# Kernel optimization log

Hardware: AMD Instinct MI355X
Metric: run time of the kernel (lower is better)

## Reference

```python
import jax, jax.numpy as jnp
import numpy as np

B, N, D, H = 1, 4096, 1024, 16
HD = D // H  # head_dim = 64


def setup_inputs() -> dict:
    key = jax.random.key(0)
    ks = jax.random.split(key, 5)
    s = 0.02
    return {
        "x": jax.random.normal(ks[0], (B, N, D), dtype=jnp.float32),
        "Wq": jax.random.normal(ks[1], (D, D), dtype=jnp.float32) * s,
        "Wk": jax.random.normal(ks[2], (D, D), dtype=jnp.float32) * s,
        "Wv": jax.random.normal(ks[3], (D, D), dtype=jnp.float32) * s,
        "Wo": jax.random.normal(ks[4], (D, D), dtype=jnp.float32) * s,
        "bo": jnp.zeros((D,), dtype=jnp.float32),
    }


def reference(x, Wq, Wk, Wv, Wo, bo):
    b, n, d = x.shape
    # QKV projections -> [b, h, n, hd]
    def proj(W):
        return jnp.einsum("bnd,de->bne", x, W).reshape(b, n, H, HD).transpose(0, 2, 1, 3)
    q, k, v = proj(Wq), proj(Wk), proj(Wv)
    # Scores [b, h, n, n] with causal mask (matches masked_fill with triu(diag=1))
    scores = jnp.einsum("bhqd,bhkd->bhqk", q, k)
    causal = jnp.tril(jnp.ones((n, n), dtype=bool))
    scores = jnp.where(causal, scores, -jnp.inf)
    attn = jax.nn.softmax(scores / jnp.sqrt(jnp.float32(HD)), axis=-1)
    # dropout p=0.0 -> identity
    ctx = jnp.einsum("bhqk,bhkd->bhqd", attn, v)
    ctx = ctx.transpose(0, 2, 1, 3).reshape(b, n, d)
    return jnp.einsum("bnd,de->bne", ctx, Wo) + bo
```

## Files before the change

kernel.cpp:

```cpp
#include <hip/hip_runtime.h>


#define N_TOK 4096
#define DMODEL 1024
#define NH 16
#define HDIM 64

typedef __bf16 bf16x8 __attribute__((ext_vector_type(8)));
typedef __bf16 bf16x2v __attribute__((ext_vector_type(2)));
typedef short short4v __attribute__((ext_vector_type(4)));
typedef unsigned int uint2v __attribute__((ext_vector_type(2)));
typedef float f32x4 __attribute__((ext_vector_type(4)));

__device__ __forceinline__ unsigned short f2bf(float f) {
  unsigned u = __builtin_bit_cast(unsigned, f);
  u += 0x7FFFu + ((u >> 16) & 1u);
  return (unsigned short)(u >> 16);
}

__device__ __forceinline__ float bf2f(unsigned short u) {
  unsigned x = (unsigned)u << 16;
  return __builtin_bit_cast(float, x);
}

__device__ __forceinline__ unsigned pack2bf(float f0, float f1) {
  unsigned a = __builtin_bit_cast(unsigned, f0);
  unsigned b = __builtin_bit_cast(unsigned, f1);
  a += 0x7FFFu + ((a >> 16) & 1u);
  b += 0x7FFFu + ((b >> 16) & 1u);
  return (a >> 16) | (b & 0xFFFF0000u);
}

__device__ __forceinline__ unsigned packpk(float f0, float f1) {
#if defined(__HIP_DEVICE_COMPILE__) && __has_builtin(__builtin_amdgcn_cvt_pk_bf16_f32)
  bf16x2v r = __builtin_amdgcn_cvt_pk_bf16_f32(f0, f1);
  return __builtin_bit_cast(unsigned, r);
#else
  return pack2bf(f0, f1);
#endif
}

__device__ __forceinline__ float fast_exp2(float x) {
#if defined(__HIP_DEVICE_COMPILE__)
#if __has_builtin(__builtin_amdgcn_exp2f)
  return __builtin_amdgcn_exp2f(x);
#else
  float r;
  asm("v_exp_f32 %0, %1" : "=v"(r) : "v"(x));
  return r;
#endif
#else
  return exp2f(x);
#endif
}

__device__ __forceinline__ f32x4 mfma16x16x16(short4v a, short4v b, f32x4 c) {
#if defined(__HIP_DEVICE_COMPILE__)
#if __has_builtin(__builtin_amdgcn_mfma_f32_16x16x16bf16_1k)
  return __builtin_amdgcn_mfma_f32_16x16x16bf16_1k(a, b, c, 0, 0, 0);
#else
  asm volatile("v_mfma_f32_16x16x16_bf16 %0, %1, %2, %0\n\ts_nop 7\n\ts_nop 1"
               : "+v"(c) : "v"(a), "v"(b));
  return c;
#endif
#else
  return c;
#endif
}

__device__ __forceinline__ void gll16(const unsigned short* g, unsigned short* l) {
#if defined(__HIP_DEVICE_COMPILE__)
  __builtin_amdgcn_global_load_lds((const __attribute__((address_space(1))) void*)g,
                                   (__attribute__((address_space(3))) void*)l, 16, 0, 0);
#endif
}

__global__ __launch_bounds__(256) void prep_kernel(
    const float* __restrict__ x, unsigned short* __restrict__ xb,
    const float* __restrict__ Wq, const float* __restrict__ Wk,
    const float* __restrict__ Wv, const float* __restrict__ Wo,
    unsigned short* __restrict__ Wqt, unsigned short* __restrict__ Wkt,
    unsigned short* __restrict__ Wvt, unsigned short* __restrict__ Wot) {
  const int bx = blockIdx.x;
  if (bx < 4096) {
    const int i = (bx * 256 + threadIdx.x) * 4;
    float4 v = *(const float4*)(x + i);
    ushort4 o;
    o.x = f2bf(v.x); o.y = f2bf(v.y); o.z = f2bf(v.z); o.w = f2bf(v.w);
    *(ushort4*)(xb + i) = o;
    return;
  }
  __shared__ float t[32][33];
  const int r = bx - 4096;
  const int z = r >> 10, rem = r & 1023;
  const int by = rem >> 5, bxx = rem & 31;
  const float* src;
  unsigned short* dst;
  switch (z) {
    case 0: src = Wq; dst = Wqt; break;
    case 1: src = Wk; dst = Wkt; break;
    case 2: src = Wv; dst = Wvt; break;
    default: src = Wo; dst = Wot; break;
  }
  const int tx = threadIdx.x & 31, ty = threadIdx.x >> 5;
  const int xx = bxx * 32 + tx;
  const int y0 = by * 32;
#pragma unroll
  for (int i = 0; i < 32; i += 8) t[ty + i][tx] = src[(y0 + ty + i) * DMODEL + xx];
  __syncthreads();
  const int ox = by * 32 + tx;
  const int oy0 = bxx * 32;
#pragma unroll
  for (int i = 0; i < 32; i += 8) dst[(oy0 + ty + i) * DMODEL + ox] = f2bf(t[tx][ty + i]);
}

__global__ __launch_bounds__(256) void gemm_qkv_kernel(
    const unsigned short* __restrict__ xb,
    const unsigned short* __restrict__ Wqt, const unsigned short* __restrict__ Wkt,
    const unsigned short* __restrict__ Wvt,
    unsigned short* __restrict__ Qg, unsigned short* __restrict__ Kg,
    unsigned short* __restrict__ Vtg) {
  __shared__ unsigned short As[128 * 32];
  __shared__ unsigned short Bs[128 * 32];
  __shared__ unsigned short Tt[64 * 132];
  const int z = blockIdx.z;
  const unsigned short* Bmat = (z == 0) ? Wqt : ((z == 1) ? Wkt : Wvt);
  const int tid = threadIdx.x, lane = tid & 63, wv = tid >> 6;
  const int quad = lane >> 4, l15 = lane & 15;
  const int wm = wv >> 1, wn = wv & 1;
  const int tm0 = blockIdx.y * 128, tn0 = blockIdx.x * 128;
  const int lrow = lane >> 2, lcol = (lane & 3) * 8;
  const f32x4 zero4 = {0.f, 0.f, 0.f, 0.f};
  f32x4 acc[4][4];
#pragma unroll
  for (int i = 0; i < 4; ++i)
#pragma unroll
    for (int j = 0; j < 4; ++j) acc[i][j] = zero4;

  for (int kb = 0; kb < DMODEL; kb += 32) {
#pragma unroll
    for (int r = 0; r < 2; ++r) {
      const int row0 = r * 64 + wv * 16;
      gll16(&xb[(tm0 + row0 + lrow) * DMODEL + kb + lcol], &As[row0 * 32]);
      gll16(&Bmat[(tn0 + row0 + lrow) * DMODEL + kb + lcol], &Bs[row0 * 32]);
    }
    __syncthreads();
    bf16x8 af[4], bfr[4];
#pragma unroll
    for (int i = 0; i < 4; ++i) {
      af[i]  = *(const bf16x8*)&As[(wm * 64 + i * 16 + l15) * 32 + quad * 8];
      bfr[i] = *(const bf16x8*)&Bs[(wn * 64 + i * 16 + l15) * 32 + quad * 8];
    }
#pragma unroll
    for (int mt = 0; mt < 4; ++mt)
#pragma unroll
      for (int nt = 0; nt < 4; ++nt)
        acc[mt][nt] = __builtin_amdgcn_mfma_f32_16x16x32_bf16(af[mt], bfr[nt], acc[mt][nt], 0, 0, 0);
    __syncthreads();
  }

  const float qs = 0.125f * 1.44269504088896f;
  if (z < 2) {
#pragma unroll
    for (int mt = 0; mt < 4; ++mt)
#pragma unroll
      for (int nt = 0; nt < 4; ++nt)
#pragma unroll
        for (int r = 0; r < 4; ++r) {
          const int row = tm0 + wm * 64 + mt * 16 + quad * 4 + r;
          const int col = tn0 + wn * 64 + nt * 16 + l15;
          const float v = acc[mt][nt][r];
          const int hh = col >> 6, hd = col & 63;
          if (z == 0) Qg[(hh * N_TOK + row) * HDIM + hd] = f2bf(v * qs);
          else        Kg[(hh * N_TOK + row) * HDIM + hd] = f2bf(v);
        }
  } else {
#pragma unroll 1
    for (int p = 0; p < 2; ++p) {
      if (wn == p) {
#pragma unroll
        for (int mt = 0; mt < 4; ++mt)
#pragma unroll
          for (int nt = 0; nt < 4; ++nt) {
            const int c = nt * 16 + l15;
#pragma unroll
            for (int r = 0; r < 4; ++r)
              Tt[c * 132 + wm * 64 + mt * 16 + quad * 4 + r] = f2bf(acc[mt][nt][r]);
          }
      }
      __syncthreads();
      const int c = tid >> 2, seg = tid & 3;
      const int hh = (tn0 + p * 64) >> 6;
      unsigned short* dst = Vtg + hh * (HDIM * N_TOK) + c * N_TOK + tm0 + seg * 32;
      const unsigned short* srcp = &Tt[c * 132 + seg * 32];
#pragma unroll
      for (int j = 0; j < 4; ++j)
        *(uint4*)(dst + j * 8) = *(const uint4*)(srcp + j * 8);
      __syncthreads();
    }
  }
}

#define TRW 68

__device__ static const unsigned char T_TAB[80] = {
    7, 14, 15, 15, 21, 22, 22, 23, 23, 23, 28, 29, 29, 30, 30, 30, 31, 31, 31, 31,
    6, 12, 13, 13, 14, 18, 19, 19, 20, 20, 20, 21, 21, 22, 24, 25, 25, 26, 26, 26,
    27, 27, 27, 27, 28, 28, 28, 29, 29, 30,
    5, 10, 11, 11, 12, 16, 16, 17, 17, 17, 18, 18, 19, 24, 24, 24, 25, 25, 26,
    4, 8, 9, 9, 10, 16,
    3, 8,
    2,
    1,
    0};
__device__ static const unsigned char G_TAB[80] = {
    0, 0, 0, 1, 0, 0, 1, 0, 1, 2, 0, 0, 1, 0, 1, 2, 0, 1, 2, 3,
    0, 0, 0, 1, 1, 0, 0, 1, 0, 1, 2, 1, 2, 2, 0, 0, 1, 0, 1, 2,
    0, 1, 2, 3, 1, 2, 3, 2, 3, 3,
    0, 0, 0, 1, 1, 0, 1, 0, 1, 2, 1, 2, 2, 1, 2, 3, 2, 3, 3,
    0, 0, 0, 1, 1, 2,
    0, 1,
    0,
    0,
    0};
__device__ static const unsigned char PS_TAB[32] = {
    0, 0, 0, 0, 0, 0, 0, 0,
    0, 2, 4, 6, 8, 10, 12, 14,
    16, 19, 22, 25, 28, 31, 34, 37,
    40, 44, 48, 52, 56, 60, 64, 68};

__device__ __forceinline__ unsigned short* part_slot_ptr(
    unsigned short* poA, unsigned short* poB, int slot) {
  return (slot < 384) ? poA + (size_t)slot * 8192
                      : poB + (size_t)(slot - 384) * 8192;
}

__device__ __forceinline__ void stage_kv(
    const unsigned short* __restrict__ Kh, const unsigned short* __restrict__ Vh,
    int kv0, char* buf, int wv, int lane) {
  unsigned short* Ksb = (unsigned short*)buf;
  unsigned short* Vsb = (unsigned short*)(buf + 8192);
  const int r8 = lane >> 3, g = lane & 7;
  const int sw = ((g ^ r8) * 8);
  const int row = wv * 8;
  gll16(&Kh[(kv0 + row + r8) * HDIM + sw], &Ksb[row * 64]);
  gll16(&Vh[(row + r8) * N_TOK + kv0 + sw], &Vsb[row * 64]);
}

template <bool MASKED>
__device__ __forceinline__ void attn_step(
    int kvs, int qw, int quad, int l15,
    const unsigned short* __restrict__ Ks, const unsigned short* __restrict__ Vs,
    const bf16x8 (&qf)[2], f32x4 (&o)[4], float& l_) {
  const f32x4 zero4 = {0.f, 0.f, 0.f, 0.f};
  const int s = l15 & 7;
  const int g0 = (quad ^ s) * 8;
  f32x4 c[4];
#pragma unroll
  for (int mt = 0; mt < 4; ++mt) {
    const unsigned short* kp = &Ks[(mt * 16 + l15) * 64];
    const bf16x8 kf0 = *(const bf16x8*)(kp + g0);
    const bf16x8 kf1 = *(const bf16x8*)(kp + (g0 ^ 32));
    c[mt] = __builtin_amdgcn_mfma_f32_16x16x32_bf16(kf0, qf[0], zero4, 0, 0, 0);
    c[mt] = __builtin_amdgcn_mfma_f32_16x16x32_bf16(kf1, qf[1], c[mt], 0, 0, 0);
  }
  short4v pb[4];
  const int q = qw + l15;
  float ls = 0.f;
#pragma unroll
  for (int mt = 0; mt < 4; ++mt) {
    float p[4];
#pragma unroll
    for (int r = 0; r < 4; ++r) {
      float v = c[mt][r];
      if (MASKED) v = ((kvs + mt * 16 + quad * 4 + r) <= q) ? v : -3e38f;
      p[r] = fast_exp2(v);
    }
    ls += (p[0] + p[1]) + (p[2] + p[3]);
    uint2v w;
    w.x = packpk(p[0], p[1]);
    w.y = packpk(p[2], p[3]);
    pb[mt] = __builtin_bit_cast(short4v, w);
  }
  l_ += ls;
#pragma unroll
  for (int mt = 0; mt < 4; ++mt)
#pragma unroll
    for (int dt = 0; dt < 4; ++dt) {
      const int gv = (((2 * mt + (quad >> 1)) ^ s) * 8) + (quad & 1) * 4;
      const short4v vfx = *(const short4v*)&Vs[(dt * 16 + l15) * 64 + gv];
      o[dt] = mfma16x16x16(vfx, pb[mt], o[dt]);
    }
}

__global__ __launch_bounds__(512, 8) void attn_kernel(
    const unsigned short* __restrict__ Qg, const unsigned short* __restrict__ Kg,
    const unsigned short* __restrict__ Vtg, unsigned short* __restrict__ ctx,
    unsigned short* __restrict__ part_oA, unsigned short* __restrict__ part_oB,
    float* __restrict__ part_l) {
  __shared__ __align__(16) char smem[34816];
  const int tid = threadIdx.x, lane = tid & 63, wv = tid >> 6;
  const int quad = lane >> 4, l15 = lane & 15;

  const int xcd = blockIdx.x & 7;
  const int iblk = blockIdx.x >> 3;
  const int h = (xcd << 1) | (iblk & 1);
  const int u = iblk >> 1;
  const int t = T_TAB[u], g = G_TAB[u];
  const int ng = (t >> 3) + 1;
  const int tp1 = t + 1;
  const int gbase = tp1 / ng;
  const int grem = tp1 - gbase * ng;
  const int s0 = g * gbase + (g < grem ? g : grem);
  const int cnt = gbase + (g < grem ? 1 : 0);
  const int mlen = 2 * cnt;
  const bool multi = (t >= 8);
  const int qb = t * 128, qw = qb + wv * 16;

  const unsigned short* Qh = Qg + h * N_TOK * HDIM;
  const unsigned short* Kh = Kg + h * N_TOK * HDIM;
  const unsigned short* Vh = Vtg + h * HDIM * N_TOK;

  bf16x8 qf[2];
#pragma unroll
  for (int hh = 0; hh < 2; ++hh)
    qf[hh] = *(const bf16x8*)&Qh[(qw + l15) * HDIM + hh * 32 + quad * 8];

  const f32x4 zero4 = {0.f, 0.f, 0.f, 0.f};
  f32x4 o[4];
#pragma unroll
  for (int dt = 0; dt < 4; ++dt) o[dt] = zero4;
  float l_ = 0.f;

  const int kvbase = s0 << 7;
  stage_kv(Kh, Vh, kvbase, smem, wv, lane);
  stage_kv(Kh, Vh, kvbase + 64, smem + 16384, wv, lane);
  int cur = 0;
#pragma unroll 1
  for (int mc = 0; mc < mlen; ++mc) {
    const int kv0 = kvbase + mc * 64;
    if (mc + 1 < mlen) asm volatile("s_waitcnt vmcnt(2)" ::: "memory");
    else               asm volatile("s_waitcnt vmcnt(0)" ::: "memory");
    __builtin_amdgcn_s_barrier();
    const unsigned short* Ksb = (const unsigned short*)(smem + cur * 16384);
    const unsigned short* Vsb = (const unsigned short*)(smem + cur * 16384 + 8192);
    if (kv0 <= qw + 15) {
      __builtin_amdgcn_s_setprio(1);
      if (kv0 + 63 <= qw)
        attn_step<false>(kv0, qw, quad, l15, Ksb, Vsb, qf, o, l_);
      else
        attn_step<true>(kv0, qw, quad, l15, Ksb, Vsb, qf, o, l_);
      __builtin_amdgcn_s_setprio(0);
    }
    if (mc + 2 < mlen) {
      __builtin_amdgcn_s_barrier();
      stage_kv(Kh, Vh, kv0 + 128, smem + cur * 16384, wv, lane);
    }
    cur ^= 1;
  }
  __syncthreads();

  float* Tr = (float*)(smem + wv * (16 * TRW * 4));
  const int tq = lane >> 2, seg = lane & 3;
  if (!multi) {
    float l = l_;
    l += __shfl_xor(l, 16, 64);
    l += __shfl_xor(l, 32, 64);
    const float inv = 1.0f / l;
#pragma unroll
    for (int dt = 0; dt < 4; ++dt) {
      f32x4 v = o[dt] * inv;
      *(f32x4*)&Tr[l15 * TRW + dt * 16 + quad * 4] = v;
    }
    unsigned short* dst = &ctx[(qb + wv * 16 + tq) * DMODEL + h * HDIM + seg * 16];
    const float* src = &Tr[tq * TRW + seg * 16];
#pragma unroll
    for (int j = 0; j < 2; ++j) {
      const float* s8 = src + j * 8;
      uint4 w;
      w.x = pack2bf(s8[0], s8[1]);
      w.y = pack2bf(s8[2], s8[3]);
      w.z = pack2bf(s8[4], s8[5]);
      w.w = pack2bf(s8[6], s8[7]);
      *(uint4*)(dst + j * 8) = w;
    }
  } else {
    const int slot = h * 72 + PS_TAB[t] + g;
    float l = l_;
    l += __shfl_xor(l, 16, 64);
    l += __shfl_xor(l, 32, 64);
    if (quad == 0) part_l[slot * 128 + wv * 16 + l15] = l;
#pragma unroll
    for (int dt = 0; dt < 4; ++dt)
      *(f32x4*)&Tr[l15 * TRW + dt * 16 + quad * 4] = o[dt];
    unsigned short* dst = part_slot_ptr(part_oA, part_oB, slot) +
                          (wv * 16 + tq) * 64 + seg * 16;
    const float* src = &Tr[tq * TRW + seg * 16];
#pragma unroll
    for (int j = 0; j < 2; ++j) {
      const float* s8 = src + j * 8;
      uint4 w;
      w.x = pack2bf(s8[0], s8[1]);
      w.y = pack2bf(s8[2], s8[3]);
      w.z = pack2bf(s8[4], s8[5]);
      w.w = pack2bf(s8[6], s8[7]);
      *(uint4*)(dst + j * 8) = w;
    }
  }
}

__global__ __launch_bounds__(256) void merge_kernel(
    unsigned short* __restrict__ part_oA, unsigned short* __restrict__ part_oB,
    const float* __restrict__ part_l, unsigned short* __restrict__ ctx) {
  const int b = blockIdx.x;
  const int h = b / 24, tt = b - h * 24;
  const int t = tt + 8;
  const int ng = (t >> 3) + 1;
  const int tid = threadIdx.x;
  const int q = tid >> 1, half = tid & 1;
  const int slot0 = h * 72 + PS_TAB[t];
  float l = 0.f;
  for (int g = 0; g < ng; ++g) l += part_l[(slot0 + g) * 128 + q];
  const float inv = 1.0f / l;
  unsigned short* dst = &ctx[(t * 128 + q) * DMODEL + h * HDIM + half * 32];
#pragma unroll
  for (int j = 0; j < 4; ++j) {
    float acc[8] = {0.f, 0.f, 0.f, 0.f, 0.f, 0.f, 0.f, 0.f};
    for (int g = 0; g < ng; ++g) {
      const unsigned short* po = part_slot_ptr(part_oA, part_oB, slot0 + g);
      const uint4 w = *(const uint4*)(po + q * 64 + half * 32 + j * 8);
      const unsigned short* us = (const unsigned short*)&w;
#pragma unroll
      for (int e = 0; e < 8; ++e) acc[e] += bf2f(us[e]);
    }
    uint4 w;
    w.x = pack2bf(acc[0] * inv, acc[1] * inv);
    w.y = pack2bf(acc[2] * inv, acc[3] * inv);
    w.z = pack2bf(acc[4] * inv, acc[5] * inv);
    w.w = pack2bf(acc[6] * inv, acc[7] * inv);
    *(uint4*)(dst + j * 8) = w;
  }
}

__global__ __launch_bounds__(256) void gemm_out_kernel(
    const unsigned short* __restrict__ ctxb, const unsigned short* __restrict__ Wot,
    const float* __restrict__ bo, float* __restrict__ out) {
  __shared__ unsigned short As[128 * 32];
  __shared__ unsigned short Bs[128 * 32];
  const int tid = threadIdx.x, lane = tid & 63, wv = tid >> 6;
  const int quad = lane >> 4, l15 = lane & 15;
  const int wm = wv >> 1, wn = wv & 1;
  const int tm0 = blockIdx.y * 128, tn0 = blockIdx.x * 128;
  const int lrow = lane >> 2, lcol = (lane & 3) * 8;
  const f32x4 zero4 = {0.f, 0.f, 0.f, 0.f};
  f32x4 acc[4][4];
#pragma unroll
  for (int i = 0; i < 4; ++i)
#pragma unroll
    for (int j = 0; j < 4; ++j) acc[i][j] = zero4;

  for (int kb = 0; kb < DMODEL; kb += 32) {
#pragma unroll
    for (int r = 0; r < 2; ++r) {
      const int row0 = r * 64 + wv * 16;
      gll16(&ctxb[(tm0 + row0 + lrow) * DMODEL + kb + lcol], &As[row0 * 32]);
      gll16(&Wot[(tn0 + row0 + lrow) * DMODEL + kb + lcol], &Bs[row0 * 32]);
    }
    __syncthreads();
    bf16x8 af[4], bfr[4];
#pragma unroll
    for (int i = 0; i < 4; ++i) {
      af[i]  = *(const bf16x8*)&As[(wm * 64 + i * 16 + l15) * 32 + quad * 8];
      bfr[i] = *(const bf16x8*)&Bs[(wn * 64 + i * 16 + l15) * 32 + quad * 8];
    }
#pragma unroll
    for (int mt = 0; mt < 4; ++mt)
#pragma unroll
      for (int nt = 0; nt < 4; ++nt)
        acc[mt][nt] = __builtin_amdgcn_mfma_f32_16x16x32_bf16(af[mt], bfr[nt], acc[mt][nt], 0, 0, 0);
    __syncthreads();
  }
#pragma unroll
  for (int mt = 0; mt < 4; ++mt)
#pragma unroll
    for (int nt = 0; nt < 4; ++nt)
#pragma unroll
      for (int r = 0; r < 4; ++r) {
        const int row = tm0 + wm * 64 + mt * 16 + quad * 4 + r;
        const int col = tn0 + wn * 64 + nt * 16 + l15;
        out[row * DMODEL + col] = acc[mt][nt][r] + bo[col];
      }
}

extern "C" void kernel_launch(void* const* d_in, const int* in_sizes, int n_in,
                              void* d_out, int out_size, void* d_ws, size_t ws_size,
                              hipStream_t stream) {
  const float* x  = (const float*)d_in[0];
  const float* Wq = (const float*)d_in[1];
  const float* Wk = (const float*)d_in[2];
  const float* Wv = (const float*)d_in[3];
  const float* Wo = (const float*)d_in[4];
  const float* bo = (const float*)d_in[5];
  float* out = (float*)d_out;

  char* ws = (char*)d_ws;
  unsigned short* xb  = (unsigned short*)(ws);
  unsigned short* Wqt = (unsigned short*)(ws + 8388608);
  unsigned short* Wkt = (unsigned short*)(ws + 8388608 + 2097152);
  unsigned short* Wvt = (unsigned short*)(ws + 8388608 + 2 * 2097152);
  unsigned short* Wot = (unsigned short*)(ws + 8388608 + 3 * 2097152);
  unsigned short* Qg  = (unsigned short*)(ws + 16777216);
  unsigned short* Kg  = (unsigned short*)(ws + 25165824);
  unsigned short* Vtg = (unsigned short*)(ws + 33554432);
  unsigned short* ctx = xb;
  unsigned short* part_oA = (unsigned short*)(ws + 8388608);
  unsigned short* part_oB = (unsigned short*)(ws + 41943040);
  float* part_l = (float*)(ws + 54525952);

  prep_kernel<<<8192, 256, 0, stream>>>(x, xb, Wq, Wk, Wv, Wo, Wqt, Wkt, Wvt, Wot);
  gemm_qkv_kernel<<<dim3(DMODEL / 128, N_TOK / 128, 3), 256, 0, stream>>>(xb, Wqt, Wkt, Wvt, Qg, Kg, Vtg);
  attn_kernel<<<1280, 512, 0, stream>>>(Qg, Kg, Vtg, ctx, part_oA, part_oB, part_l);
  merge_kernel<<<384, 256, 0, stream>>>(part_oA, part_oB, part_l, ctx);
  gemm_out_kernel<<<dim3(DMODEL / 128, N_TOK / 128), 256, 0, stream>>>(ctx, Wot, bo, out);
}
```

Before: 232.9 us.

## Process two 16-row query tiles per wave to double K/V reuse in attention

Each wave now handles 32 query rows (two 16-row MFMA tiles) instead of 16, so every K and V fragment read from LDS feeds two MFMA chains. The query block per workgroup grows to 256 rows, which halves the attention grid and forces the split-KV tables, partial slot layout and merge kernel to be rebuilt for 16 query tiles per head. This cuts LDS traffic and staging per unit of work but raises register pressure (launch bounds drop from 8 to 4 waves per SIMD), leaves fewer blocks for load balancing, and makes masking coarser.

```diff
diff --git a/kernel.cpp b/kernel.cpp
--- a/kernel.cpp
+++ b/kernel.cpp
@@ -203,36 +203,30 @@
 
 #define TRW 68
 
-__device__ static const unsigned char T_TAB[80] = {
-    7, 14, 15, 15, 21, 22, 22, 23, 23, 23, 28, 29, 29, 30, 30, 30, 31, 31, 31, 31,
-    6, 12, 13, 13, 14, 18, 19, 19, 20, 20, 20, 21, 21, 22, 24, 25, 25, 26, 26, 26,
-    27, 27, 27, 27, 28, 28, 28, 29, 29, 30,
-    5, 10, 11, 11, 12, 16, 16, 17, 17, 17, 18, 18, 19, 24, 24, 24, 25, 25, 26,
-    4, 8, 9, 9, 10, 16,
-    3, 8,
-    2,
+__device__ static const unsigned char T_TAB[40] = {
+    3, 7, 7, 10, 11, 11, 11, 14, 14, 15, 15, 15, 15,
+    6, 6, 9, 9, 10, 10, 12, 12, 13, 13, 13, 13, 14, 14,
+    2, 5, 5, 8, 8, 8, 9, 12, 12,
+    4, 4,
     1,
     0};
-__device__ static const unsigned char G_TAB[80] = {
-    0, 0, 0, 1, 0, 0, 1, 0, 1, 2, 0, 0, 1, 0, 1, 2, 0, 1, 2, 3,
-    0, 0, 0, 1, 1, 0, 0, 1, 0, 1, 2, 1, 2, 2, 0, 0, 1, 0, 1, 2,
-    0, 1, 2, 3, 1, 2, 3, 2, 3, 3,
-    0, 0, 0, 1, 1, 0, 1, 0, 1, 2, 1, 2, 2, 1, 2, 3, 2, 3, 3,
-    0, 0, 0, 1, 1, 2,
+__device__ static const unsigned char G_TAB[40] = {
+    0, 0, 1, 0, 0, 1, 2, 0, 1, 0, 1, 2, 3,
+    0, 1, 0, 1, 1, 2, 0, 1, 0, 1, 2, 3, 2, 3,
+    0, 0, 1, 0, 1, 2, 2, 2, 3,
     0, 1,
     0,
-    0,
     0};
-__device__ static const unsigned char PS_TAB[32] = {
-    0, 0, 0, 0, 0, 0, 0, 0,
-    0, 2, 4, 6, 8, 10, 12, 14,
-    16, 19, 22, 25, 28, 31, 34, 37,
-    40, 44, 48, 52, 56, 60, 64, 68};
+__device__ static const unsigned char PS_TAB[16] = {
+    0, 0, 0, 0,
+    0, 2, 4, 6,
+    8, 11, 14, 17,
+    20, 24, 28, 32};
 
 __device__ __forceinline__ unsigned short* part_slot_ptr(
     unsigned short* poA, unsigned short* poB, int slot) {
-  return (slot < 384) ? poA + (size_t)slot * 8192
-                      : poB + (size_t)(slot - 384) * 8192;
+  return (slot < 192) ? poA + (size_t)slot * 16384
+                      : poB + (size_t)(slot - 192) * 16384;
 }
 
 __device__ __forceinline__ void stage_kv(
@@ -251,49 +245,56 @@
 __device__ __forceinline__ void attn_step(
     int kvs, int qw, int quad, int l15,
     const unsigned short* __restrict__ Ks, const unsigned short* __restrict__ Vs,
-    const bf16x8 (&qf)[2], f32x4 (&o)[4], float& l_) {
+    const bf16x8 (&qf)[2][2], f32x4 (&o)[2][4], float (&l_)[2]) {
   const f32x4 zero4 = {0.f, 0.f, 0.f, 0.f};
   const int s = l15 & 7;
-  const int g0 = (quad ^ s) * 8;
-  f32x4 c[4];
+  f32x4 c[2][4];
 #pragma unroll
   for (int mt = 0; mt < 4; ++mt) {
     const unsigned short* kp = &Ks[(mt * 16 + l15) * 64];
+    const int g0 = (quad ^ s) * 8;
     const bf16x8 kf0 = *(const bf16x8*)(kp + g0);
     const bf16x8 kf1 = *(const bf16x8*)(kp + (g0 ^ 32));
-    c[mt] = __builtin_amdgcn_mfma_f32_16x16x32_bf16(kf0, qf[0], zero4, 0, 0, 0);
-    c[mt] = __builtin_amdgcn_mfma_f32_16x16x32_bf16(kf1, qf[1], c[mt], 0, 0, 0);
-  }
-  short4v pb[4];
-  const int q = qw + l15;
-  float ls = 0.f;
-#pragma unroll
-  for (int mt = 0; mt < 4; ++mt) {
-    float p[4];
-#pragma unroll
-    for (int r = 0; r < 4; ++r) {
-      float v = c[mt][r];
-      if (MASKED) v = ((kvs + mt * 16 + quad * 4 + r) <= q) ? v : -3e38f;
-      p[r] = fast_exp2(v);
-    }
-    ls += (p[0] + p[1]) + (p[2] + p[3]);
-    uint2v w;
-    w.x = packpk(p[0], p[1]);
-    w.y = packpk(p[2], p[3]);
-    pb[mt] = __builtin_bit_cast(short4v, w);
-  }
-  l_ += ls;
+#pragma unroll
+    for (int qt = 0; qt < 2; ++qt) {
+      c[qt][mt] = __builtin_amdgcn_mfma_f32_16x16x32_bf16(kf0, qf[qt][0], zero4, 0, 0, 0);
+      c[qt][mt] = __builtin_amdgcn_mfma_f32_16x16x32_bf16(kf1, qf[qt][1], c[qt][mt], 0, 0, 0);
+    }
+  }
+  short4v pb[2][4];
+#pragma unroll
+  for (int qt = 0; qt < 2; ++qt) {
+    const int q = qw + qt * 16 + l15;
+    float ls = 0.f;
+#pragma unroll
+    for (int mt = 0; mt < 4; ++mt) {
+      float p[4];
+#pragma unroll
+      for (int r = 0; r < 4; ++r) {
+        float v = c[qt][mt][r];
+        if (MASKED) v = ((kvs + mt * 16 + quad * 4 + r) <= q) ? v : -3e38f;
+        p[r] = fast_exp2(v);
+      }
+      ls += (p[0] + p[1]) + (p[2] + p[3]);
+      uint2v w;
+      w.x = packpk(p[0], p[1]);
+      w.y = packpk(p[2], p[3]);
+      pb[qt][mt] = __builtin_bit_cast(short4v, w);
+    }
+    l_[qt] += ls;
+  }
 #pragma unroll
   for (int mt = 0; mt < 4; ++mt)
 #pragma unroll
     for (int dt = 0; dt < 4; ++dt) {
       const int gv = (((2 * mt + (quad >> 1)) ^ s) * 8) + (quad & 1) * 4;
       const short4v vfx = *(const short4v*)&Vs[(dt * 16 + l15) * 64 + gv];
-      o[dt] = mfma16x16x16(vfx, pb[mt], o[dt]);
-    }
-}
-
-__global__ __launch_bounds__(512, 8) void attn_kernel(
+      o[0][dt] = mfma16x16x16(vfx, pb[0][mt], o[0][dt]);
+      o[1][dt] = mfma16x16x16(vfx, pb[1][mt], o[1][dt]);
+    }
+}
+
+__global__ __launch_bounds__(512, 4) void attn_kernel(
     const unsigned short* __restrict__ Qg, const unsigned short* __restrict__ Kg,
     const unsigned short* __restrict__ Vtg, unsigned short* __restrict__ ctx,
     unsigned short* __restrict__ part_oA, unsigned short* __restrict__ part_oB,
@@ -307,30 +308,34 @@
   const int h = (xcd << 1) | (iblk & 1);
   const int u = iblk >> 1;
   const int t = T_TAB[u], g = G_TAB[u];
-  const int ng = (t >> 3) + 1;
-  const int tp1 = t + 1;
-  const int gbase = tp1 / ng;
-  const int grem = tp1 - gbase * ng;
+  const int ng = (t >> 2) + 1;
+  const int M = 2 * t + 2;
+  const int gbase = M / ng;
+  const int grem = M - gbase * ng;
   const int s0 = g * gbase + (g < grem ? g : grem);
   const int cnt = gbase + (g < grem ? 1 : 0);
   const int mlen = 2 * cnt;
-  const bool multi = (t >= 8);
-  const int qb = t * 128, qw = qb + wv * 16;
+  const bool multi = (t >= 4);
+  const int qb = t * 256, qw = qb + wv * 32;
 
   const unsigned short* Qh = Qg + h * N_TOK * HDIM;
   const unsigned short* Kh = Kg + h * N_TOK * HDIM;
   const unsigned short* Vh = Vtg + h * HDIM * N_TOK;
 
-  bf16x8 qf[2];
-#pragma unroll
-  for (int hh = 0; hh < 2; ++hh)
-    qf[hh] = *(const bf16x8*)&Qh[(qw + l15) * HDIM + hh * 32 + quad * 8];
+  bf16x8 qf[2][2];
+#pragma unroll
+  for (int qt = 0; qt < 2; ++qt)
+#pragma unroll
+    for (int hh = 0; hh < 2; ++hh)
+      qf[qt][hh] = *(const bf16x8*)&Qh[(qw + qt * 16 + l15) * HDIM + hh * 32 + quad * 8];
 
   const f32x4 zero4 = {0.f, 0.f, 0.f, 0.f};
-  f32x4 o[4];
-#pragma unroll
-  for (int dt = 0; dt < 4; ++dt) o[dt] = zero4;
-  float l_ = 0.f;
+  f32x4 o[2][4];
+#pragma unroll
+  for (int qt = 0; qt < 2; ++qt)
+#pragma unroll
+    for (int dt = 0; dt < 4; ++dt) o[qt][dt] = zero4;
+  float l_[2] = {0.f, 0.f};
 
   const int kvbase = s0 << 7;
   stage_kv(Kh, Vh, kvbase, smem, wv, lane);
@@ -344,7 +349,7 @@
     __builtin_amdgcn_s_barrier();
     const unsigned short* Ksb = (const unsigned short*)(smem + cur * 16384);
     const unsigned short* Vsb = (const unsigned short*)(smem + cur * 16384 + 8192);
-    if (kv0 <= qw + 15) {
+    if (kv0 <= qw + 31) {
       __builtin_amdgcn_s_setprio(1);
       if (kv0 + 63 <= qw)
         attn_step<false>(kv0, qw, quad, l15, Ksb, Vsb, qf, o, l_);
@@ -363,66 +368,72 @@
   float* Tr = (float*)(smem + wv * (16 * TRW * 4));
   const int tq = lane >> 2, seg = lane & 3;
   if (!multi) {
-    float l = l_;
-    l += __shfl_xor(l, 16, 64);
-    l += __shfl_xor(l, 32, 64);
-    const float inv = 1.0f / l;
-#pragma unroll
-    for (int dt = 0; dt < 4; ++dt) {
-      f32x4 v = o[dt] * inv;
-      *(f32x4*)&Tr[l15 * TRW + dt * 16 + quad * 4] = v;
-    }
-    unsigned short* dst = &ctx[(qb + wv * 16 + tq) * DMODEL + h * HDIM + seg * 16];
-    const float* src = &Tr[tq * TRW + seg * 16];
-#pragma unroll
-    for (int j = 0; j < 2; ++j) {
-      const float* s8 = src + j * 8;
-      uint4 w;
-      w.x = pack2bf(s8[0], s8[1]);
-      w.y = pack2bf(s8[2], s8[3]);
-      w.z = pack2bf(s8[4], s8[5]);
-      w.w = pack2bf(s8[6], s8[7]);
-      *(uint4*)(dst + j * 8) = w;
+#pragma unroll 1
+    for (int qt = 0; qt < 2; ++qt) {
+      float l = l_[qt];
+      l += __shfl_xor(l, 16, 64);
+      l += __shfl_xor(l, 32, 64);
+      const float inv = 1.0f / l;
+#pragma unroll
+      for (int dt = 0; dt < 4; ++dt) {
+        f32x4 v = o[qt][dt] * inv;
+        *(f32x4*)&Tr[l15 * TRW + dt * 16 + quad * 4] = v;
+      }
+      unsigned short* dst = &ctx[(qb + wv * 32 + qt * 16 + tq) * DMODEL + h * HDIM + seg * 16];
+      const float* src = &Tr[tq * TRW + seg * 16];
+#pragma unroll
+      for (int j = 0; j < 2; ++j) {
+        const float* s8 = src + j * 8;
+        uint4 w;
+        w.x = pack2bf(s8[0], s8[1]);
+        w.y = pack2bf(s8[2], s8[3]);
+        w.z = pack2bf(s8[4], s8[5]);
+        w.w = pack2bf(s8[6], s8[7]);
+        *(uint4*)(dst + j * 8) = w;
+      }
     }
   } else {
-    const int slot = h * 72 + PS_TAB[t] + g;
-    float l = l_;
-    l += __shfl_xor(l, 16, 64);
-    l += __shfl_xor(l, 32, 64);
-    if (quad == 0) part_l[slot * 128 + wv * 16 + l15] = l;
-#pragma unroll
-    for (int dt = 0; dt < 4; ++dt)
-      *(f32x4*)&Tr[l15 * TRW + dt * 16 + quad * 4] = o[dt];
-    unsigned short* dst = part_slot_ptr(part_oA, part_oB, slot) +
-                          (wv * 16 + tq) * 64 + seg * 16;
-    const float* src = &Tr[tq * TRW + seg * 16];
-#pragma unroll
-    for (int j = 0; j < 2; ++j) {
-      const float* s8 = src + j * 8;
-      uint4 w;
-      w.x = pack2bf(s8[0], s8[1]);
-      w.y = pack2bf(s8[2], s8[3]);
-      w.z = pack2bf(s8[4], s8[5]);
-      w.w = pack2bf(s8[6], s8[7]);
-      *(uint4*)(dst + j * 8) = w;
-    }
-  }
-}
-
-__global__ __launch_bounds__(256) void merge_kernel(
+    const int slot = h * 36 + PS_TAB[t] + g;
+    unsigned short* pobase = part_slot_ptr(part_oA, part_oB, slot);
+#pragma unroll 1
+    for (int qt = 0; qt < 2; ++qt) {
+      float l = l_[qt];
+      l += __shfl_xor(l, 16, 64);
+      l += __shfl_xor(l, 32, 64);
+      if (quad == 0) part_l[slot * 256 + wv * 32 + qt * 16 + l15] = l;
+#pragma unroll
+      for (int dt = 0; dt < 4; ++dt)
+        *(f32x4*)&Tr[l15 * TRW + dt * 16 + quad * 4] = o[qt][dt];
+      unsigned short* dst = pobase + (wv * 32 + qt * 16 + tq) * 64 + seg * 16;
+      const float* src = &Tr[tq * TRW + seg * 16];
+#pragma unroll
+      for (int j = 0; j < 2; ++j) {
+        const float* s8 = src + j * 8;
+        uint4 w;
+        w.x = pack2bf(s8[0], s8[1]);
+        w.y = pack2bf(s8[2], s8[3]);
+        w.z = pack2bf(s8[4], s8[5]);
+        w.w = pack2bf(s8[6], s8[7]);
+        *(uint4*)(dst + j * 8) = w;
+      }
+    }
+  }
+}
+
+__global__ __launch_bounds__(512) void merge_kernel(
     unsigned short* __restrict__ part_oA, unsigned short* __restrict__ part_oB,
     const float* __restrict__ part_l, unsigned short* __restrict__ ctx) {
   const int b = blockIdx.x;
-  const int h = b / 24, tt = b - h * 24;
-  const int t = tt + 8;
-  const int ng = (t >> 3) + 1;
+  const int h = b / 12, tt = b - h * 12;
+  const int t = tt + 4;
+  const int ng = (t >> 2) + 1;
   const int tid = threadIdx.x;
   const int q = tid >> 1, half = tid & 1;
-  const int slot0 = h * 72 + PS_TAB[t];
+  const int slot0 = h * 36 + PS_TAB[t];
   float l = 0.f;
-  for (int g = 0; g < ng; ++g) l += part_l[(slot0 + g) * 128 + q];
+  for (int g = 0; g < ng; ++g) l += part_l[(slot0 + g) * 256 + q];
   const float inv = 1.0f / l;
-  unsigned short* dst = &ctx[(t * 128 + q) * DMODEL + h * HDIM + half * 32];
+  unsigned short* dst = &ctx[(t * 256 + q) * DMODEL + h * HDIM + half * 32];
 #pragma unroll
   for (int j = 0; j < 4; ++j) {
     float acc[8] = {0.f, 0.f, 0.f, 0.f, 0.f, 0.f, 0.f, 0.f};
@@ -519,7 +530,7 @@
 
   prep_kernel<<<8192, 256, 0, stream>>>(x, xb, Wq, Wk, Wv, Wo, Wqt, Wkt, Wvt, Wot);
   gemm_qkv_kernel<<<dim3(DMODEL / 128, N_TOK / 128, 3), 256, 0, stream>>>(xb, Wqt, Wkt, Wvt, Qg, Kg, Vtg);
-  attn_kernel<<<1280, 512, 0, stream>>>(Qg, Kg, Vtg, ctx, part_oA, part_oB, part_l);
-  merge_kernel<<<384, 256, 0, stream>>>(part_oA, part_oB, part_l, ctx);
+  attn_kernel<<<640, 512, 0, stream>>>(Qg, Kg, Vtg, ctx, part_oA, part_oB, part_l);
+  merge_kernel<<<192, 512, 0, stream>>>(part_oA, part_oB, part_l, ctx);
   gemm_out_kernel<<<dim3(DMODEL / 128, N_TOK / 128), 256, 0, stream>>>(ctx, Wot, bo, out);
 }
```

Result: slower. 243.9 us (+4.7%).

## Give each attention wave two 16-row query tiles, sharing K/V fragments

Applied to the files above, without the earlier changes.

Halves the attention block to 4 waves of 256 threads, with each wave handling 32 query rows (two 16-row tiles) instead of 16. Each K and V fragment read from LDS now feeds two MFMAs, which halves LDS read traffic per unit of compute. Each wave stages twice as many K/V rows, and the vmcnt wait is raised to match. The cost is more registers per wave and fewer waves to hide latency. Causal skipping is also coarser at 32-row granularity, so more masked work runs.

```diff
diff --git a/kernel.cpp b/kernel.cpp
--- a/kernel.cpp
+++ b/kernel.cpp
@@ -242,58 +242,68 @@
   unsigned short* Vsb = (unsigned short*)(buf + 8192);
   const int r8 = lane >> 3, g = lane & 7;
   const int sw = ((g ^ r8) * 8);
-  const int row = wv * 8;
-  gll16(&Kh[(kv0 + row + r8) * HDIM + sw], &Ksb[row * 64]);
-  gll16(&Vh[(row + r8) * N_TOK + kv0 + sw], &Vsb[row * 64]);
+#pragma unroll
+  for (int i = 0; i < 2; ++i) {
+    const int row = wv * 16 + i * 8;
+    gll16(&Kh[(kv0 + row + r8) * HDIM + sw], &Ksb[row * 64]);
+    gll16(&Vh[(row + r8) * N_TOK + kv0 + sw], &Vsb[row * 64]);
+  }
 }
 
 template <bool MASKED>
 __device__ __forceinline__ void attn_step(
     int kvs, int qw, int quad, int l15,
     const unsigned short* __restrict__ Ks, const unsigned short* __restrict__ Vs,
-    const bf16x8 (&qf)[2], f32x4 (&o)[4], float& l_) {
+    const bf16x8 (&qf)[2][2], f32x4 (&o)[2][4], float (&l_)[2]) {
   const f32x4 zero4 = {0.f, 0.f, 0.f, 0.f};
   const int s = l15 & 7;
-  const int g0 = (quad ^ s) * 8;
-  f32x4 c[4];
+  f32x4 c[2][4];
 #pragma unroll
   for (int mt = 0; mt < 4; ++mt) {
     const unsigned short* kp = &Ks[(mt * 16 + l15) * 64];
+    const int g0 = (quad ^ s) * 8;
     const bf16x8 kf0 = *(const bf16x8*)(kp + g0);
     const bf16x8 kf1 = *(const bf16x8*)(kp + (g0 ^ 32));
-    c[mt] = __builtin_amdgcn_mfma_f32_16x16x32_bf16(kf0, qf[0], zero4, 0, 0, 0);
-    c[mt] = __builtin_amdgcn_mfma_f32_16x16x32_bf16(kf1, qf[1], c[mt], 0, 0, 0);
-  }
-  short4v pb[4];
-  const int q = qw + l15;
-  float ls = 0.f;
-#pragma unroll
-  for (int mt = 0; mt < 4; ++mt) {
-    float p[4];
-#pragma unroll
-    for (int r = 0; r < 4; ++r) {
-      float v = c[mt][r];
-      if (MASKED) v = ((kvs + mt * 16 + quad * 4 + r) <= q) ? v : -3e38f;
-      p[r] = fast_exp2(v);
-    }
-    ls += (p[0] + p[1]) + (p[2] + p[3]);
-    uint2v w;
-    w.x = packpk(p[0], p[1]);
-    w.y = packpk(p[2], p[3]);
-    pb[mt] = __builtin_bit_cast(short4v, w);
-  }
-  l_ += ls;
+#pragma unroll
+    for (int qt = 0; qt < 2; ++qt) {
+      c[qt][mt] = __builtin_amdgcn_mfma_f32_16x16x32_bf16(kf0, qf[qt][0], zero4, 0, 0, 0);
+      c[qt][mt] = __builtin_amdgcn_mfma_f32_16x16x32_bf16(kf1, qf[qt][1], c[qt][mt], 0, 0, 0);
+    }
+  }
+  short4v pb[2][4];
+#pragma unroll
+  for (int qt = 0; qt < 2; ++qt) {
+    const int q = qw + qt * 16 + l15;
+    float ls = 0.f;
+#pragma unroll
+    for (int mt = 0; mt < 4; ++mt) {
+      float p[4];
+#pragma unroll
+      for (int r = 0; r < 4; ++r) {
+        float v = c[qt][mt][r];
+        if (MASKED) v = ((kvs + mt * 16 + quad * 4 + r) <= q) ? v : -3e38f;
+        p[r] = fast_exp2(v);
+      }
+      ls += (p[0] + p[1]) + (p[2] + p[3]);
+      uint2v w;
+      w.x = packpk(p[0], p[1]);
+      w.y = packpk(p[2], p[3]);
+      pb[qt][mt] = __builtin_bit_cast(short4v, w);
+    }
+    l_[qt] += ls;
+  }
 #pragma unroll
   for (int mt = 0; mt < 4; ++mt)
 #pragma unroll
     for (int dt = 0; dt < 4; ++dt) {
       const int gv = (((2 * mt + (quad >> 1)) ^ s) * 8) + (quad & 1) * 4;
       const short4v vfx = *(const short4v*)&Vs[(dt * 16 + l15) * 64 + gv];
-      o[dt] = mfma16x16x16(vfx, pb[mt], o[dt]);
-    }
-}
-
-__global__ __launch_bounds__(512, 8) void attn_kernel(
+      o[0][dt] = mfma16x16x16(vfx, pb[0][mt], o[0][dt]);
+      o[1][dt] = mfma16x16x16(vfx, pb[1][mt], o[1][dt]);
+    }
+}
+
+__global__ __launch_bounds__(256, 4) void attn_kernel(
     const unsigned short* __restrict__ Qg, const unsigned short* __restrict__ Kg,
     const unsigned short* __restrict__ Vtg, unsigned short* __restrict__ ctx,
     unsigned short* __restrict__ part_oA, unsigned short* __restrict__ part_oB,
@@ -315,22 +325,26 @@
   const int cnt = gbase + (g < grem ? 1 : 0);
   const int mlen = 2 * cnt;
   const bool multi = (t >= 8);
-  const int qb = t * 128, qw = qb + wv * 16;
+  const int qb = t * 128, qw = qb + wv * 32;
 
   const unsigned short* Qh = Qg + h * N_TOK * HDIM;
   const unsigned short* Kh = Kg + h * N_TOK * HDIM;
   const unsigned short* Vh = Vtg + h * HDIM * N_TOK;
 
-  bf16x8 qf[2];
-#pragma unroll
-  for (int hh = 0; hh < 2; ++hh)
-    qf[hh] = *(const bf16x8*)&Qh[(qw + l15) * HDIM + hh * 32 + quad * 8];
+  bf16x8 qf[2][2];
+#pragma unroll
+  for (int qt = 0; qt < 2; ++qt)
+#pragma unroll
+    for (int hh = 0; hh < 2; ++hh)
+      qf[qt][hh] = *(const bf16x8*)&Qh[(qw + qt * 16 + l15) * HDIM + hh * 32 + quad * 8];
 
   const f32x4 zero4 = {0.f, 0.f, 0.f, 0.f};
-  f32x4 o[4];
-#pragma unroll
-  for (int dt = 0; dt < 4; ++dt) o[dt] = zero4;
-  float l_ = 0.f;
+  f32x4 o[2][4];
+#pragma unroll
+  for (int qt = 0; qt < 2; ++qt)
+#pragma unroll
+    for (int dt = 0; dt < 4; ++dt) o[qt][dt] = zero4;
+  float l_[2] = {0.f, 0.f};
 
   const int kvbase = s0 << 7;
   stage_kv(Kh, Vh, kvbase, smem, wv, lane);
@@ -339,12 +353,12 @@
 #pragma unroll 1
   for (int mc = 0; mc < mlen; ++mc) {
     const int kv0 = kvbase + mc * 64;
-    if (mc + 1 < mlen) asm volatile("s_waitcnt vmcnt(2)" ::: "memory");
+    if (mc + 1 < mlen) asm volatile("s_waitcnt vmcnt(4)" ::: "memory");
     else               asm volatile("s_waitcnt vmcnt(0)" ::: "memory");
     __builtin_amdgcn_s_barrier();
     const unsigned short* Ksb = (const unsigned short*)(smem + cur * 16384);
     const unsigned short* Vsb = (const unsigned short*)(smem + cur * 16384 + 8192);
-    if (kv0 <= qw + 15) {
+    if (kv0 <= qw + 31) {
       __builtin_amdgcn_s_setprio(1);
       if (kv0 + 63 <= qw)
         attn_step<false>(kv0, qw, quad, l15, Ksb, Vsb, qf, o, l_);
@@ -363,48 +377,54 @@
   float* Tr = (float*)(smem + wv * (16 * TRW * 4));
   const int tq = lane >> 2, seg = lane & 3;
   if (!multi) {
-    float l = l_;
-    l += __shfl_xor(l, 16, 64);
-    l += __shfl_xor(l, 32, 64);
-    const float inv = 1.0f / l;
-#pragma unroll
-    for (int dt = 0; dt < 4; ++dt) {
-      f32x4 v = o[dt] * inv;
-      *(f32x4*)&Tr[l15 * TRW + dt * 16 + quad * 4] = v;
-    }
-    unsigned short* dst = &ctx[(qb + wv * 16 + tq) * DMODEL + h * HDIM + seg * 16];
-    const float* src = &Tr[tq * TRW + seg * 16];
-#pragma unroll
-    for (int j = 0; j < 2; ++j) {
-      const float* s8 = src + j * 8;
-      uint4 w;
-      w.x = pack2bf(s8[0], s8[1]);
-      w.y = pack2bf(s8[2], s8[3]);
-      w.z = pack2bf(s8[4], s8[5]);
-      w.w = pack2bf(s8[6], s8[7]);
-      *(uint4*)(dst + j * 8) = w;
+#pragma unroll
+    for (int qt = 0; qt < 2; ++qt) {
+      float l = l_[qt];
+      l += __shfl_xor(l, 16, 64);
+      l += __shfl_xor(l, 32, 64);
+      const float inv = 1.0f / l;
+#pragma unroll
+      for (int dt = 0; dt < 4; ++dt) {
+        f32x4 v = o[qt][dt] * inv;
+        *(f32x4*)&Tr[l15 * TRW + dt * 16 + quad * 4] = v;
+      }
+      unsigned short* dst = &ctx[(qb + wv * 32 + qt * 16 + tq) * DMODEL + h * HDIM + seg * 16];
+      const float* src = &Tr[tq * TRW + seg * 16];
+#pragma unroll
+      for (int j = 0; j < 2; ++j) {
+        const float* s8 = src + j * 8;
+        uint4 w;
+        w.x = pack2bf(s8[0], s8[1]);
+        w.y = pack2bf(s8[2], s8[3]);
+        w.z = pack2bf(s8[4], s8[5]);
+        w.w = pack2bf(s8[6], s8[7]);
+        *(uint4*)(dst + j * 8) = w;
+      }
     }
   } else {
     const int slot = h * 72 + PS_TAB[t] + g;
-    float l = l_;
-    l += __shfl_xor(l, 16, 64);
-    l += __shfl_xor(l, 32, 64);
-    if (quad == 0) part_l[slot * 128 + wv * 16 + l15] = l;
-#pragma unroll
-    for (int dt = 0; dt < 4; ++dt)
-      *(f32x4*)&Tr[l15 * TRW + dt * 16 + quad * 4] = o[dt];
-    unsigned short* dst = part_slot_ptr(part_oA, part_oB, slot) +
-                          (wv * 16 + tq) * 64 + seg * 16;
-    const float* src = &Tr[tq * TRW + seg * 16];
-#pragma unroll
-    for (int j = 0; j < 2; ++j) {
-      const float* s8 = src + j * 8;
-      uint4 w;
-      w.x = pack2bf(s8[0], s8[1]);
-      w.y = pack2bf(s8[2], s8[3]);
-      w.z = pack2bf(s8[4], s8[5]);
-      w.w = pack2bf(s8[6], s8[7]);
-      *(uint4*)(dst + j * 8) = w;
+    unsigned short* pobase = part_slot_ptr(part_oA, part_oB, slot);
+#pragma unroll
+    for (int qt = 0; qt < 2; ++qt) {
+      float l = l_[qt];
+      l += __shfl_xor(l, 16, 64);
+      l += __shfl_xor(l, 32, 64);
+      if (quad == 0) part_l[slot * 128 + wv * 32 + qt * 16 + l15] = l;
+#pragma unroll
+      for (int dt = 0; dt < 4; ++dt)
+        *(f32x4*)&Tr[l15 * TRW + dt * 16 + quad * 4] = o[qt][dt];
+      unsigned short* dst = pobase + (wv * 32 + qt * 16 + tq) * 64 + seg * 16;
+      const float* src = &Tr[tq * TRW + seg * 16];
+#pragma unroll
+      for (int j = 0; j < 2; ++j) {
+        const float* s8 = src + j * 8;
+        uint4 w;
+        w.x = pack2bf(s8[0], s8[1]);
+        w.y = pack2bf(s8[2], s8[3]);
+        w.z = pack2bf(s8[4], s8[5]);
+        w.w = pack2bf(s8[6], s8[7]);
+        *(uint4*)(dst + j * 8) = w;
+      }
     }
   }
 }
@@ -519,7 +539,7 @@
 
   prep_kernel<<<8192, 256, 0, stream>>>(x, xb, Wq, Wk, Wv, Wo, Wqt, Wkt, Wvt, Wot);
   gemm_qkv_kernel<<<dim3(DMODEL / 128, N_TOK / 128, 3), 256, 0, stream>>>(xb, Wqt, Wkt, Wvt, Qg, Kg, Vtg);
-  attn_kernel<<<1280, 512, 0, stream>>>(Qg, Kg, Vtg, ctx, part_oA, part_oB, part_l);
+  attn_kernel<<<1280, 256, 0, stream>>>(Qg, Kg, Vtg, ctx, part_oA, part_oB, part_l);
   merge_kernel<<<384, 256, 0, stream>>>(part_oA, part_oB, part_l, ctx);
   gemm_out_kernel<<<dim3(DMODEL / 128, N_TOK / 128), 256, 0, stream>>>(ctx, Wot, bo, out);
 }
```

Result: faster. 220.5 us (-5.3%).
